# Kernel tuning notes

Hardware: AMD Instinct MI355X
Metric: run time of the kernel (lower is better)

## Reference

```python
import jax, jax.numpy as jnp
import numpy as np
from jax import lax

B, IMG, CIN, C, HEADS, K = 2, 112, 64, 256, 8, 3  # kernel_size[0]=3 used by hatt1
HD = C // HEADS


def layer_norm(x, w, b, eps=1e-5):
    mu = jnp.mean(x, axis=-1, keepdims=True)
    var = jnp.mean((x - mu) ** 2, axis=-1, keepdims=True)
    return (x - mu) / jnp.sqrt(var + eps) * w + b


def conv3x3(x, w, b):
    # x: (B,Cin,H,W), w: (Cout,Cin,3,3) -- stride 1, pad 1 (OverlapPatchEmbed patchsize=3)
    y = lax.conv_general_dilated(x, w, (1, 1), ((1, 1), (1, 1)),
                                 dimension_numbers=('NCHW', 'OIHW', 'NCHW'))
    return y + b[None, :, None, None]


def nat_cross_attention(q_in, kv_in, wq, bq, wkv, bkv, rpb, wp, bp, heads=HEADS, k=K):
    # NATTEN-style 2D neighborhood attention with separate query / key-value maps.
    Bb, H, W, Cc = q_in.shape
    hd = Cc // heads
    scale = hd ** -0.5
    q = (q_in @ wq + bq).reshape(Bb, H, W, heads, hd) * scale
    kv = (kv_in @ wkv + bkv).reshape(Bb, H, W, 2, heads, hd)
    kk, v = kv[:, :, :, 0], kv[:, :, :, 1]
    half = k // 2
    # border-clamped window starts -> every pixel attends to a full k x k window
    si = jnp.clip(jnp.arange(H) - half, 0, H - k)  # (H,)
    sj = jnp.clip(jnp.arange(W) - half, 0, W - k)  # (W,)
    nbi = si[:, None] + jnp.arange(k)  # (H,k) neighbor rows
    nbj = sj[:, None] + jnp.arange(k)  # (W,k) neighbor cols

    def gather(t):  # t: (B,H,W,heads,hd) -> (B,H,W,heads,k*k,hd)
        g = t[:, nbi]            # (B,H,k,W,heads,hd)
        g = g[:, :, :, nbj]      # (B,H,k,W,k,heads,hd)
        return jnp.transpose(g, (0, 1, 3, 5, 2, 4, 6)).reshape(Bb, H, W, heads, k * k, hd)

    kg, vg = gather(kk), gather(v)
    logits = jnp.einsum('bijhd,bijhnd->bijhn', q, kg)
    # relative position bias: rpb (heads, 2k-1, 2k-1)
    pi = jnp.arange(H) - si  # query position inside its window, 0..k-1
    pj = jnp.arange(W) - sj
    idx_i = jnp.arange(k)[None, :] - pi[:, None] + (k - 1)  # (H,k) in [0, 2k-2]
    idx_j = jnp.arange(k)[None, :] - pj[:, None] + (k - 1)  # (W,k)
    bias = rpb[:, idx_i]           # (heads,H,k,2k-1)
    bias = bias[:, :, :, idx_j]    # (heads,H,k,W,k)
    bias = jnp.transpose(bias, (1, 3, 0, 2, 4)).reshape(H, W, heads, k * k)
    attn = jax.nn.softmax(logits + bias, axis=-1)
    out = jnp.einsum('bijhn,bijhnd->bijhd', attn, vg).reshape(Bb, H, W, Cc)
    return out @ wp + bp


def setup_inputs() -> dict:
    key = jax.random.key(0)
    ks = jax.random.split(key, 24)
    std = 0.02
    inp = {
        'xq': jax.random.normal(ks[0], (B, CIN, IMG, IMG), jnp.float32),
        'xkv': jax.random.normal(ks[1], (B, CIN, IMG, IMG), jnp.float32),
        'conv1_w': jax.random.normal(ks[2], (C, CIN, 3, 3), jnp.float32) * std,
        'conv1_b': jnp.zeros((C,), jnp.float32),
        'conv3_w': jax.random.normal(ks[3], (C, CIN, 3, 3), jnp.float32) * std,
        'conv3_b': jnp.zeros((C,), jnp.float32),
        'ln1_w': jnp.ones((C,), jnp.float32), 'ln1_b': jnp.zeros((C,), jnp.float32),
        'ln10_w': jnp.ones((C,), jnp.float32), 'ln10_b': jnp.zeros((C,), jnp.float32),
        'ln3_w': jnp.ones((C,), jnp.float32), 'ln3_b': jnp.zeros((C,), jnp.float32),
        'wq': jax.random.normal(ks[4], (C, C), jnp.float32) * std,
        'bq': jnp.zeros((C,), jnp.float32),
        'wkv': jax.random.normal(ks[5], (C, 2 * C), jnp.float32) * std,
        'bkv': jnp.zeros((2 * C,), jnp.float32),
        'rpb': jax.random.normal(ks[6], (HEADS, 2 * K - 1, 2 * K - 1), jnp.float32) * std,
        'wp': jax.random.normal(ks[7], (C, C), jnp.float32) * std,
        'bp': jnp.zeros((C,), jnp.float32),
        'fc1_w': jax.random.normal(ks[8], (C, 2 * C), jnp.float32) * std,
        'fc1_b': jnp.zeros((2 * C,), jnp.float32),
        'fc2_w': jax.random.normal(ks[9], (2 * C, C), jnp.float32) * std,
        'fc2_b': jnp.zeros((C,), jnp.float32),
    }
    return inp


def reference(xq, xkv, conv1_w, conv1_b, conv3_w, conv3_b, ln1_w, ln1_b, ln10_w, ln10_b,
              ln3_w, ln3_b, wq, bq, wkv, bkv, rpb, wp, bp, fc1_w, fc1_b, fc2_w, fc2_b):
    # patch embeds (stride-1 3x3 conv, pad 1), channels-last maps (B,H,W,C)
    x1 = jnp.transpose(conv3x3(xq, conv1_w, conv1_b), (0, 2, 3, 1))
    x3 = jnp.transpose(conv3x3(xkv, conv3_w, conv3_b), (0, 2, 3, 1))
    qn = layer_norm(x1, ln1_w, ln1_b)    # norm1(x_embedding1)
    kvn = layer_norm(x1, ln10_w, ln10_b)  # norm1_0(x_embedding1)
    att1 = nat_cross_attention(qn, kvn, wq, bq, wkv, bkv, rpb, wp, bp)
    att = att1 + x3  # drop_path is identity at inference
    h = layer_norm(att, ln3_w, ln3_b)
    m = jax.nn.gelu(h @ fc1_w + fc1_b, approximate=False) @ fc2_w + fc2_b
    x = m + att
    return jnp.transpose(x, (0, 3, 1, 2))  # (B,C,H,W)
```

## Files before the change

### kernel.cpp

```cpp
#include <hip/hip_runtime.h>
#include <math.h>

#define IMG 112
#define CIN 64
#define CH 256
#define PADW 114
#define IMG2 12544
#define NPIX 25088

typedef __bf16 bf16;
typedef __bf16 bf16x4 __attribute__((ext_vector_type(4)));
typedef __bf16 bf16x8 __attribute__((ext_vector_type(8)));
typedef float f32x4 __attribute__((ext_vector_type(4)));

__device__ __forceinline__ void gld_lds16(const void* g, void* l) {
    __builtin_amdgcn_global_load_lds(
        (const __attribute__((address_space(1))) void*)g,
        (__attribute__((address_space(3))) void*)l,
        16, 0, 0);
}

__global__ __launch_bounds__(256) void pad_nhwc_kernel(const float* __restrict__ in, bf16* __restrict__ out) {
    int bi = blockIdx.x;
    int b = bi / IMG, i = bi % IMG;
    __shared__ float lds[CIN * 113];
    const float* src = in + (size_t)b * CIN * IMG2 + (size_t)i * IMG;
    for (int t = threadIdx.x; t < CIN * IMG; t += 256) {
        int ci = t / IMG, j = t - ci * IMG;
        lds[ci * 113 + j] = src[(size_t)ci * IMG2 + j];
    }
    __syncthreads();
    bf16* dst = out + (((size_t)(b * PADW + (i + 1)) * PADW) + 1) * CIN;
    for (int t = threadIdx.x; t < CIN * IMG; t += 256) {
        int j = t / CIN, ci = t - j * CIN;
        dst[(size_t)j * CIN + ci] = (bf16)lds[ci * 113 + j];
    }
}

__global__ __launch_bounds__(256) void convw_kernel(const float* __restrict__ w1, const float* __restrict__ w2,
                                                    bf16* __restrict__ o1, bf16* __restrict__ o2) {
    int idx = blockIdx.x * 256 + threadIdx.x;
    if (idx >= CH * 576) return;
    int co = idx / 576, r = idx - co * 576;
    int tap = r >> 6, ci = r & 63;
    int src = co * 576 + ci * 9 + tap;
    o1[idx] = (bf16)w1[src];
    o2[idx] = (bf16)w2[src];
}

__global__ __launch_bounds__(256) void transw_kernel(const float* __restrict__ in, bf16* __restrict__ out,
                                                     int K, int N, float scale) {
    int idx = blockIdx.x * 256 + threadIdx.x;
    if (idx >= N * K) return;
    int n = idx / K, k = idx - n * K;
    out[idx] = (bf16)(in[(size_t)k * N + n] * scale);
}

template <int NOUT>
__global__ __launch_bounds__(256) void ln_kernel(
    const float* __restrict__ x,
    const float* __restrict__ w0, const float* __restrict__ b0, bf16* __restrict__ o0,
    const float* __restrict__ w1, const float* __restrict__ b1, bf16* __restrict__ o1) {
    int row = blockIdx.x * 4 + (threadIdx.x >> 6);
    int lane = threadIdx.x & 63;
    const float* xr = x + (size_t)row * CH + lane * 4;
    f32x4 v = *(const f32x4*)xr;
    float s = v[0] + v[1] + v[2] + v[3];
    float ss = v[0] * v[0] + v[1] * v[1] + v[2] * v[2] + v[3] * v[3];
#pragma unroll
    for (int off = 32; off > 0; off >>= 1) {
        s += __shfl_xor(s, off);
        ss += __shfl_xor(ss, off);
    }
    float mean = s * (1.0f / CH);
    float rstd = rsqrtf(ss * (1.0f / CH) - mean * mean + 1e-5f);
    int c = lane * 4;
    {
        f32x4 w = *(const f32x4*)(w0 + c);
        f32x4 bb = *(const f32x4*)(b0 + c);
        bf16x4 o;
#pragma unroll
        for (int e = 0; e < 4; ++e) o[e] = (bf16)((v[e] - mean) * rstd * w[e] + bb[e]);
        *(bf16x4*)(o0 + (size_t)row * CH + c) = o;
    }
    if (NOUT == 2) {
        f32x4 w = *(const f32x4*)(w1 + c);
        f32x4 bb = *(const f32x4*)(b1 + c);
        bf16x4 o;
#pragma unroll
        for (int e = 0; e < 4; ++e) o[e] = (bf16)((v[e] - mean) * rstd * w[e] + bb[e]);
        *(bf16x4*)(o1 + (size_t)row * CH + c) = o;
    }
}

template <int AMODE, int EPI>
__global__ __launch_bounds__(256) void gemm_kernel(
    const bf16* __restrict__ A, const bf16* __restrict__ Bt,
    const float* __restrict__ bias, float biasScale,
    const float* __restrict__ res,
    float* __restrict__ outf, bf16* __restrict__ outb,
    int N, int K) {
    __shared__ __align__(16) bf16 As[128 * 64];
    __shared__ __align__(16) bf16 Bs[128 * 64];
    const int tid = threadIdx.x;
    const int wave = tid >> 6, lane = tid & 63;
    const int m0 = blockIdx.x * 128, n0 = blockIdx.y * 128;
    const int wm = wave >> 1, wn = wave & 1;
    const int fr = lane & 15, fq = lane >> 4;
    const int srow = wave * 32 + (lane >> 3);
    const int scol = (lane & 7) * 8;

    const bf16* aptr[4];
    const bf16* bptr[4];
#pragma unroll
    for (int q = 0; q < 4; ++q) {
        int arow = m0 + srow + q * 8;
        if (AMODE == 1) {
            int b = arow / IMG2;
            int rem = arow - b * IMG2;
            int i = rem / IMG, j = rem - i * IMG;
            aptr[q] = A + ((size_t)((b * PADW + i) * PADW + j)) * CIN + scol;
        } else {
            aptr[q] = A + (size_t)arow * K + scol;
        }
        bptr[q] = Bt + (size_t)(n0 + srow + q * 8) * K + scol;
    }

    f32x4 acc[4][4] = {};
    const int nk = K >> 6;
    for (int kt = 0; kt < nk; ++kt) {
        int aoff;
        if (AMODE == 1) {
            int di = kt / 3, dj = kt - di * 3;
            aoff = (di * PADW + dj) * CIN;
        } else {
            aoff = kt * 64;
        }
        int boff = kt * 64;
#pragma unroll
        for (int q = 0; q < 4; ++q) {
            gld_lds16(aptr[q] + aoff, &As[(wave * 4 + q) * 512]);
            gld_lds16(bptr[q] + boff, &Bs[(wave * 4 + q) * 512]);
        }
        __syncthreads();
#pragma unroll
        for (int ks = 0; ks < 2; ++ks) {
            bf16x8 af[4], bfr[4];
#pragma unroll
            for (int mi = 0; mi < 4; ++mi)
                af[mi] = *(const bf16x8*)&As[(wm * 64 + mi * 16 + fr) * 64 + ks * 32 + fq * 8];
#pragma unroll
            for (int ni = 0; ni < 4; ++ni)
                bfr[ni] = *(const bf16x8*)&Bs[(wn * 64 + ni * 16 + fr) * 64 + ks * 32 + fq * 8];
#pragma unroll
            for (int mi = 0; mi < 4; ++mi)
#pragma unroll
                for (int ni = 0; ni < 4; ++ni)
                    acc[mi][ni] = __builtin_amdgcn_mfma_f32_16x16x32_bf16(af[mi], bfr[ni], acc[mi][ni], 0, 0, 0);
        }
        __syncthreads();
    }

#pragma unroll
    for (int mi = 0; mi < 4; ++mi) {
#pragma unroll
        for (int ni = 0; ni < 4; ++ni) {
            int col = n0 + wn * 64 + ni * 16 + fr;
            float bv = (EPI & 1) ? bias[col] * biasScale : 0.0f;
#pragma unroll
            for (int r = 0; r < 4; ++r) {
                int prow = m0 + wm * 64 + mi * 16 + fq * 4 + r;
                float x = acc[mi][ni][r] + bv;
                if (EPI & 2) x = 0.5f * x * (1.0f + erff(x * 0.70710678118f));
                if (EPI & 4) x += res[(size_t)prow * N + col];
                if (EPI & 8) outf[(size_t)prow * N + col] = x;
                if (EPI & 16) outb[(size_t)prow * N + col] = (bf16)x;
                if (EPI & 32) {
                    int b = prow / IMG2;
                    int rem = prow - b * IMG2;
                    int ii = rem / IMG, jj = rem - ii * IMG;
                    outf[(((size_t)b * CH + col) * IMG + ii) * IMG + jj] = x;
                }
            }
        }
    }
}

__global__ __launch_bounds__(256) void attn_kernel(const bf16* __restrict__ q, const bf16* __restrict__ kv,
                                                   const float* __restrict__ rpb, bf16* __restrict__ out) {
    int idx = blockIdx.x * 256 + threadIdx.x;
    int h = idx & 7, p = idx >> 3;
    int b = p / IMG2;
    int rem = p - b * IMG2;
    int i = rem / IMG, j = rem - i * IMG;
    int si = i - 1; if (si < 0) si = 0; if (si > IMG - 3) si = IMG - 3;
    int sj = j - 1; if (sj < 0) sj = 0; if (sj > IMG - 3) sj = IMG - 3;
    int pi = i - si, pj = j - sj;

    float qv[32];
    {
        const bf16x8* qp = (const bf16x8*)(q + (size_t)p * CH + h * 32);
#pragma unroll
        for (int g = 0; g < 4; ++g) {
            bf16x8 t = qp[g];
#pragma unroll
            for (int e = 0; e < 8; ++e) qv[g * 8 + e] = (float)t[e];
        }
    }
    float logits[9];
#pragma unroll
    for (int a = 0; a < 3; ++a) {
#pragma unroll
        for (int bb = 0; bb < 3; ++bb) {
            int pn = (b * IMG + (si + a)) * IMG + (sj + bb);
            const bf16x8* kp = (const bf16x8*)(kv + (size_t)pn * 512 + h * 32);
            float s = 0.0f;
#pragma unroll
            for (int g = 0; g < 4; ++g) {
                bf16x8 t = kp[g];
#pragma unroll
                for (int e = 0; e < 8; ++e) s += qv[g * 8 + e] * (float)t[e];
            }
            logits[a * 3 + bb] = s + rpb[(h * 5 + (a - pi + 2)) * 5 + (bb - pj + 2)];
        }
    }
    float mx = logits[0];
#pragma unroll
    for (int n = 1; n < 9; ++n) mx = fmaxf(mx, logits[n]);
    float den = 0.0f;
#pragma unroll
    for (int n = 0; n < 9; ++n) { logits[n] = expf(logits[n] - mx); den += logits[n]; }
    float inv = 1.0f / den;
    float o[32] = {};
#pragma unroll
    for (int a = 0; a < 3; ++a) {
#pragma unroll
        for (int bb = 0; bb < 3; ++bb) {
            int pn = (b * IMG + (si + a)) * IMG + (sj + bb);
            float wgt = logits[a * 3 + bb] * inv;
            const bf16x8* vp = (const bf16x8*)(kv + (size_t)pn * 512 + 256 + h * 32);
#pragma unroll
            for (int g = 0; g < 4; ++g) {
                bf16x8 t = vp[g];
#pragma unroll
                for (int e = 0; e < 8; ++e) o[g * 8 + e] += wgt * (float)t[e];
            }
        }
    }
    bf16* op = out + (size_t)p * CH + h * 32;
#pragma unroll
    for (int g = 0; g < 4; ++g) {
        bf16x8 t;
#pragma unroll
        for (int e = 0; e < 8; ++e) t[e] = (bf16)o[g * 8 + e];
        *(bf16x8*)(op + g * 8) = t;
    }
}

extern "C" void kernel_launch(void* const* d_in, const int* in_sizes, int n_in,
                              void* d_out, int out_size, void* d_ws, size_t ws_size,
                              hipStream_t stream) {
    (void)in_sizes; (void)n_in; (void)out_size; (void)ws_size;
    const float* xq    = (const float*)d_in[0];
    const float* xkv   = (const float*)d_in[1];
    const float* c1w   = (const float*)d_in[2];
    const float* c1b   = (const float*)d_in[3];
    const float* c3w   = (const float*)d_in[4];
    const float* c3b   = (const float*)d_in[5];
    const float* ln1w  = (const float*)d_in[6];
    const float* ln1b  = (const float*)d_in[7];
    const float* ln10w = (const float*)d_in[8];
    const float* ln10b = (const float*)d_in[9];
    const float* ln3w  = (const float*)d_in[10];
    const float* ln3b  = (const float*)d_in[11];
    const float* wq    = (const float*)d_in[12];
    const float* bq    = (const float*)d_in[13];
    const float* wkv   = (const float*)d_in[14];
    const float* bkv   = (const float*)d_in[15];
    const float* rpb   = (const float*)d_in[16];
    const float* wp    = (const float*)d_in[17];
    const float* bp    = (const float*)d_in[18];
    const float* f1w   = (const float*)d_in[19];
    const float* f1b   = (const float*)d_in[20];
    const float* f2w   = (const float*)d_in[21];
    const float* f2b   = (const float*)d_in[22];
    float* out = (float*)d_out;

    char* ws = (char*)d_ws;
    bf16*  PADQ  = (bf16*)(ws + 0);
    bf16*  PADKV = (bf16*)(ws + 3326976);
    bf16*  CW1   = (bf16*)(ws + 6653952);
    bf16*  CW2   = (bf16*)(ws + 6948864);
    bf16*  WQT   = (bf16*)(ws + 7243776);
    bf16*  WKVT  = (bf16*)(ws + 7374848);
    bf16*  WPT   = (bf16*)(ws + 7636992);
    bf16*  WF1   = (bf16*)(ws + 7768064);
    bf16*  WF2   = (bf16*)(ws + 8030208);
    float* X1    = (float*)(ws + 8292352);
    bf16*  KV    = (bf16*)(ws + 8292352);
    float* X3    = (float*)(ws + 33982464);
    bf16*  QN    = (bf16*)(ws + 59672576);
    bf16*  M1    = (bf16*)(ws + 59672576);
    bf16*  KVN   = (bf16*)(ws + 72517632);
    bf16*  Q     = (bf16*)(ws + 85362688);
    bf16*  H     = (bf16*)(ws + 85362688);
    bf16*  AO    = (bf16*)(ws + 98207744);
    float* ATT   = (float*)(ws + 111052800);

    const float SC = 0.17677669529663687f;

    hipMemsetAsync(PADQ, 0, 6653952, stream);
    pad_nhwc_kernel<<<224, 256, 0, stream>>>(xq, PADQ);
    pad_nhwc_kernel<<<224, 256, 0, stream>>>(xkv, PADKV);
    convw_kernel<<<576, 256, 0, stream>>>(c1w, c3w, CW1, CW2);
    transw_kernel<<<256, 256, 0, stream>>>(wq, WQT, 256, 256, SC);
    transw_kernel<<<512, 256, 0, stream>>>(wkv, WKVT, 256, 512, 1.0f);
    transw_kernel<<<256, 256, 0, stream>>>(wp, WPT, 256, 256, 1.0f);
    transw_kernel<<<512, 256, 0, stream>>>(f1w, WF1, 256, 512, 1.0f);
    transw_kernel<<<512, 256, 0, stream>>>(f2w, WF2, 512, 256, 1.0f);

    dim3 g2(196, 2), g4(196, 4);
    gemm_kernel<1, 1 | 8><<<g2, 256, 0, stream>>>(PADQ, CW1, c1b, 1.0f, nullptr, X1, nullptr, 256, 576);
    gemm_kernel<1, 1 | 8><<<g2, 256, 0, stream>>>(PADKV, CW2, c3b, 1.0f, nullptr, X3, nullptr, 256, 576);
    ln_kernel<2><<<6272, 256, 0, stream>>>(X1, ln1w, ln1b, QN, ln10w, ln10b, KVN);
    gemm_kernel<0, 1 | 16><<<g2, 256, 0, stream>>>(QN, WQT, bq, SC, nullptr, nullptr, Q, 256, 256);
    gemm_kernel<0, 1 | 16><<<g4, 256, 0, stream>>>(KVN, WKVT, bkv, 1.0f, nullptr, nullptr, KV, 512, 256);
    attn_kernel<<<784, 256, 0, stream>>>(Q, KV, rpb, AO);
    gemm_kernel<0, 1 | 4 | 8><<<g2, 256, 0, stream>>>(AO, WPT, bp, 1.0f, X3, ATT, nullptr, 256, 256);
    ln_kernel<1><<<6272, 256, 0, stream>>>(ATT, ln3w, ln3b, H, nullptr, nullptr, nullptr);
    gemm_kernel<0, 1 | 2 | 16><<<g4, 256, 0, stream>>>(H, WF1, f1b, 1.0f, nullptr, nullptr, M1, 512, 256);
    gemm_kernel<0, 1 | 4 | 32><<<g2, 256, 0, stream>>>(M1, WF2, f2b, 1.0f, ATT, out, nullptr, 256, 512);
}
```

Before: 327.9 us.

## Shrink GEMM tiles to 64x64 with double-buffered LDS and XOR swizzle

The shared GEMM kernel moves from 128x128 to 64x64 output tiles, which quadruples the grid to give the CUs more blocks and better occupancy (launch bounds hint 5 blocks per CU). It double-buffers LDS so the next K-slice's global-to-LDS loads overlap the current slice's MFMAs, and XOR-swizzles LDS columns to avoid bank conflicts on fragment reads. The cost is lower arithmetic intensity per tile, with more global traffic for A and B reloads, and an explicit vmcnt wait plus barrier per iteration.

New measurement: 298.3 us. -9.0%, faster.

```diff
diff --git a/kernel.cpp b/kernel.cpp
--- a/kernel.cpp
+++ b/kernel.cpp
@@ -19,6 +19,9 @@
         (__attribute__((address_space(3))) void*)l,
         16, 0, 0);
 }
+
+#define VMCNT0() asm volatile("s_waitcnt vmcnt(0)" ::: "memory")
+#define BAR() __builtin_amdgcn_s_barrier()
 
 __global__ __launch_bounds__(256) void pad_nhwc_kernel(const float* __restrict__ in, bf16* __restrict__ out) {
     int bi = blockIdx.x;
@@ -94,27 +97,29 @@
 }
 
 template <int AMODE, int EPI>
-__global__ __launch_bounds__(256) void gemm_kernel(
+__global__ __launch_bounds__(256, 5) void gemm_kernel(
     const bf16* __restrict__ A, const bf16* __restrict__ Bt,
     const float* __restrict__ bias, float biasScale,
     const float* __restrict__ res,
     float* __restrict__ outf, bf16* __restrict__ outb,
     int N, int K) {
-    __shared__ __align__(16) bf16 As[128 * 64];
-    __shared__ __align__(16) bf16 Bs[128 * 64];
+    __shared__ __align__(16) bf16 As[2][64 * 64];
+    __shared__ __align__(16) bf16 Bs[2][64 * 64];
     const int tid = threadIdx.x;
     const int wave = tid >> 6, lane = tid & 63;
-    const int m0 = blockIdx.x * 128, n0 = blockIdx.y * 128;
+    const int m0 = blockIdx.x * 64, n0 = blockIdx.y * 64;
     const int wm = wave >> 1, wn = wave & 1;
     const int fr = lane & 15, fq = lane >> 4;
-    const int srow = wave * 32 + (lane >> 3);
-    const int scol = (lane & 7) * 8;
-
-    const bf16* aptr[4];
-    const bf16* bptr[4];
-#pragma unroll
-    for (int q = 0; q < 4; ++q) {
-        int arow = m0 + srow + q * 8;
+
+    const int srow = (lane >> 3);
+    const int swzc = (lane & 7) ^ srow;
+    const int scol = swzc * 8;
+
+    const bf16* aptr[2];
+    const bf16* bptr[2];
+#pragma unroll
+    for (int q = 0; q < 2; ++q) {
+        int arow = m0 + wave * 16 + q * 8 + srow;
         if (AMODE == 1) {
             int b = arow / IMG2;
             int rem = arow - b * IMG2;
@@ -123,12 +128,10 @@
         } else {
             aptr[q] = A + (size_t)arow * K + scol;
         }
-        bptr[q] = Bt + (size_t)(n0 + srow + q * 8) * K + scol;
-    }
-
-    f32x4 acc[4][4] = {};
-    const int nk = K >> 6;
-    for (int kt = 0; kt < nk; ++kt) {
+        bptr[q] = Bt + (size_t)(n0 + wave * 16 + q * 8 + srow) * K + scol;
+    }
+
+    auto STAGE = [&](int bufi, int kt) {
         int aoff;
         if (AMODE == 1) {
             int di = kt / 3, dj = kt - di * 3;
@@ -137,39 +140,57 @@
             aoff = kt * 64;
         }
         int boff = kt * 64;
-#pragma unroll
-        for (int q = 0; q < 4; ++q) {
-            gld_lds16(aptr[q] + aoff, &As[(wave * 4 + q) * 512]);
-            gld_lds16(bptr[q] + boff, &Bs[(wave * 4 + q) * 512]);
-        }
-        __syncthreads();
+        gld_lds16(aptr[0] + aoff, &As[bufi][(wave * 16 + 0) * 64]);
+        gld_lds16(aptr[1] + aoff, &As[bufi][(wave * 16 + 8) * 64]);
+        gld_lds16(bptr[0] + boff, &Bs[bufi][(wave * 16 + 0) * 64]);
+        gld_lds16(bptr[1] + boff, &Bs[bufi][(wave * 16 + 8) * 64]);
+    };
+
+    f32x4 acc[2][2] = {};
+    const int sw = fr & 7;
+    const int aR[2] = { (wm * 32 + fr) * 64, (wm * 32 + 16 + fr) * 64 };
+    const int bR[2] = { (wn * 32 + fr) * 64, (wn * 32 + 16 + fr) * 64 };
+
+    auto COMPUTE = [&](int bufi) {
 #pragma unroll
         for (int ks = 0; ks < 2; ++ks) {
-            bf16x8 af[4], bfr[4];
-#pragma unroll
-            for (int mi = 0; mi < 4; ++mi)
-                af[mi] = *(const bf16x8*)&As[(wm * 64 + mi * 16 + fr) * 64 + ks * 32 + fq * 8];
-#pragma unroll
-            for (int ni = 0; ni < 4; ++ni)
-                bfr[ni] = *(const bf16x8*)&Bs[(wn * 64 + ni * 16 + fr) * 64 + ks * 32 + fq * 8];
-#pragma unroll
-            for (int mi = 0; mi < 4; ++mi)
-#pragma unroll
-                for (int ni = 0; ni < 4; ++ni)
-                    acc[mi][ni] = __builtin_amdgcn_mfma_f32_16x16x32_bf16(af[mi], bfr[ni], acc[mi][ni], 0, 0, 0);
-        }
-        __syncthreads();
-    }
-
-#pragma unroll
-    for (int mi = 0; mi < 4; ++mi) {
-#pragma unroll
-        for (int ni = 0; ni < 4; ++ni) {
-            int col = n0 + wn * 64 + ni * 16 + fr;
+            int ch = (ks * 4 + fq) ^ sw;
+            bf16x8 af[2], bv[2];
+#pragma unroll
+            for (int mi = 0; mi < 2; ++mi) af[mi] = *(const bf16x8*)&As[bufi][aR[mi] + ch * 8];
+#pragma unroll
+            for (int ni = 0; ni < 2; ++ni) bv[ni] = *(const bf16x8*)&Bs[bufi][bR[ni] + ch * 8];
+#pragma unroll
+            for (int mi = 0; mi < 2; ++mi)
+#pragma unroll
+                for (int ni = 0; ni < 2; ++ni)
+                    acc[mi][ni] = __builtin_amdgcn_mfma_f32_16x16x32_bf16(af[mi], bv[ni], acc[mi][ni], 0, 0, 0);
+        }
+    };
+
+    const int nk = K >> 6;
+    STAGE(0, 0);
+    VMCNT0();
+    BAR();
+    int cur = 0;
+    for (int kt = 0; kt < nk - 1; ++kt) {
+        STAGE(cur ^ 1, kt + 1);
+        COMPUTE(cur);
+        VMCNT0();
+        BAR();
+        cur ^= 1;
+    }
+    COMPUTE(cur);
+
+#pragma unroll
+    for (int mi = 0; mi < 2; ++mi) {
+#pragma unroll
+        for (int ni = 0; ni < 2; ++ni) {
+            int col = n0 + wn * 32 + ni * 16 + fr;
             float bv = (EPI & 1) ? bias[col] * biasScale : 0.0f;
 #pragma unroll
             for (int r = 0; r < 4; ++r) {
-                int prow = m0 + wm * 64 + mi * 16 + fq * 4 + r;
+                int prow = m0 + wm * 32 + mi * 16 + fq * 4 + r;
                 float x = acc[mi][ni][r] + bv;
                 if (EPI & 2) x = 0.5f * x * (1.0f + erff(x * 0.70710678118f));
                 if (EPI & 4) x += res[(size_t)prow * N + col];
@@ -319,15 +340,15 @@
     transw_kernel<<<512, 256, 0, stream>>>(f1w, WF1, 256, 512, 1.0f);
     transw_kernel<<<512, 256, 0, stream>>>(f2w, WF2, 512, 256, 1.0f);
 
-    dim3 g2(196, 2), g4(196, 4);
-    gemm_kernel<1, 1 | 8><<<g2, 256, 0, stream>>>(PADQ, CW1, c1b, 1.0f, nullptr, X1, nullptr, 256, 576);
-    gemm_kernel<1, 1 | 8><<<g2, 256, 0, stream>>>(PADKV, CW2, c3b, 1.0f, nullptr, X3, nullptr, 256, 576);
+    dim3 g4(392, 4), g8(392, 8);
+    gemm_kernel<1, 1 | 8><<<g4, 256, 0, stream>>>(PADQ, CW1, c1b, 1.0f, nullptr, X1, nullptr, 256, 576);
+    gemm_kernel<1, 1 | 8><<<g4, 256, 0, stream>>>(PADKV, CW2, c3b, 1.0f, nullptr, X3, nullptr, 256, 576);
     ln_kernel<2><<<6272, 256, 0, stream>>>(X1, ln1w, ln1b, QN, ln10w, ln10b, KVN);
-    gemm_kernel<0, 1 | 16><<<g2, 256, 0, stream>>>(QN, WQT, bq, SC, nullptr, nullptr, Q, 256, 256);
-    gemm_kernel<0, 1 | 16><<<g4, 256, 0, stream>>>(KVN, WKVT, bkv, 1.0f, nullptr, nullptr, KV, 512, 256);
+    gemm_kernel<0, 1 | 16><<<g4, 256, 0, stream>>>(QN, WQT, bq, SC, nullptr, nullptr, Q, 256, 256);
+    gemm_kernel<0, 1 | 16><<<g8, 256, 0, stream>>>(KVN, WKVT, bkv, 1.0f, nullptr, nullptr, KV, 512, 256);
     attn_kernel<<<784, 256, 0, stream>>>(Q, KV, rpb, AO);
-    gemm_kernel<0, 1 | 4 | 8><<<g2, 256, 0, stream>>>(AO, WPT, bp, 1.0f, X3, ATT, nullptr, 256, 256);
+    gemm_kernel<0, 1 | 4 | 8><<<g4, 256, 0, stream>>>(AO, WPT, bp, 1.0f, X3, ATT, nullptr, 256, 256);
     ln_kernel<1><<<6272, 256, 0, stream>>>(ATT, ln3w, ln3b, H, nullptr, nullptr, nullptr);
-    gemm_kernel<0, 1 | 2 | 16><<<g4, 256, 0, stream>>>(H, WF1, f1b, 1.0f, nullptr, nullptr, M1, 512, 256);
-    gemm_kernel<0, 1 | 4 | 32><<<g2, 256, 0, stream>>>(M1, WF2, f2b, 1.0f, ATT, out, nullptr, 256, 512);
-}
+    gemm_kernel<0, 1 | 2 | 16><<<g8, 256, 0, stream>>>(H, WF1, f1b, 1.0f, nullptr, nullptr, M1, 512, 256);
+    gemm_kernel<0, 1 | 4 | 32><<<g4, 256, 0, stream>>>(M1, WF2, f2b, 1.0f, ATT, out, nullptr, 256, 512);
+}
```
